# Kernel tuning notes

Measured on AMD Instinct MI355X. Metric: run time of the kernel, lower is better.

The kernel has to match this reference:

```python
import jax, jax.numpy as jnp
import numpy as np

N_HEADS = 8
D_EMBED = 512
D_HEAD = D_EMBED // N_HEADS  # used only for the scale factor, as in the source


def setup_inputs() -> dict:
    key = jax.random.key(0)
    k1, k2, k3, k4, k5 = jax.random.split(key, 5)
    B, S, D = 4, 4096, D_EMBED
    s = 1.0 / np.sqrt(D)
    return {
        "x": jax.random.normal(k1, (B, S, D), dtype=jnp.float32),
        "w_in": jax.random.normal(k2, (3 * D, D), dtype=jnp.float32) * s,
        "b_in": jax.random.normal(k3, (3 * D,), dtype=jnp.float32) * 0.01,
        "w_out": jax.random.normal(k4, (D, D), dtype=jnp.float32) * s,
        "b_out": jax.random.normal(k5, (D,), dtype=jnp.float32) * 0.01,
    }


def reference(x, w_in, b_in, w_out, b_out):
    # in_proj: torch Linear y = x @ W.T + b ; chunk into q,k,v along last dim
    qkv = jnp.einsum("bsd,ed->bse", x, w_in) + b_in  # [B,S,3D]
    q, k, v = jnp.split(qkv, 3, axis=-1)  # each [B,S,D]
    # NOTE: source never splits into heads; attention over full d_embed,
    # but scaled by sqrt(d_head) = sqrt(d_embed / n_heads).
    scores = jnp.einsum("bqd,bkd->bqk", q, k) / np.sqrt(D_HEAD)  # [B,S,S]
    weight = jax.nn.softmax(scores, axis=-1)
    out = jnp.einsum("bqk,bkd->bqd", weight, v)  # [B,S,D]
    out = jnp.einsum("bsd,ed->bse", out, w_out) + b_out
    return out
```

## Files before the change

kernel.cpp:

```cpp
#include <hip/hip_runtime.h>

typedef __bf16 bf16x8 __attribute__((ext_vector_type(8)));
typedef float f32x4 __attribute__((ext_vector_type(4)));

#define MFMA16(a, b, c) __builtin_amdgcn_mfma_f32_16x16x32_bf16(a, b, c, 0, 0, 0)
#define LOG2E 1.44269504088896340736f

__device__ __forceinline__ unsigned short f2bf(float f) {
  union { float f; unsigned u; } v; v.f = f;
  return (unsigned short)((v.u + 0x7fffu + ((v.u >> 16) & 1u)) >> 16);
}
__device__ __forceinline__ bf16x8 ld_frag(const unsigned short* p) {
  return *(const bf16x8*)p;
}
__device__ __forceinline__ void gld_lds16(const unsigned short* g, unsigned short* l) {
  __builtin_amdgcn_global_load_lds(
      (const __attribute__((address_space(1))) unsigned int*)(const void*)g,
      (__attribute__((address_space(3))) unsigned int*)(void*)l, 16, 0, 0);
}

__global__ void cvt_f2bf(const float* __restrict__ in,
                         unsigned short* __restrict__ out, int n4) {
  int i = blockIdx.x * blockDim.x + threadIdx.x;
  if (i < n4) {
    float4 v = ((const float4*)in)[i];
    ushort4 o;
    o.x = f2bf(v.x); o.y = f2bf(v.y); o.z = f2bf(v.z); o.w = f2bf(v.w);
    ((ushort4*)out)[i] = o;
  }
}

__global__ void gemm_bt(const unsigned short* __restrict__ A,
                        const unsigned short* __restrict__ B,
                        const float* __restrict__ bias,
                        float* __restrict__ outf,
                        unsigned short* __restrict__ qbuf,
                        unsigned short* __restrict__ kbuf,
                        unsigned short* __restrict__ vtbuf,
                        int M, int N, int K, int mode) {
  __shared__ alignas(16) unsigned short As[128 * 32];
  __shared__ alignas(16) unsigned short Bs[128 * 32];
  const int n0 = blockIdx.x * 128, m0 = blockIdx.y * 128;
  const int tid = threadIdx.x;
  const int l = tid & 63, w = tid >> 6;
  const int quad = l >> 4, c = l & 15;
  const int wm = (w >> 1) * 64, wn = (w & 1) * 64;

  f32x4 acc[4][4] = {};
  const int kiters = K >> 5;
  for (int kt = 0; kt < kiters; ++kt) {
    __syncthreads();
    const int kk = kt * 32 + (l & 3) * 8;
    const int row = l >> 2;
#pragma unroll
    for (int i = 0; i < 2; ++i) {
      const int rbase = i * 64 + w * 16;
      gld_lds16(&A[(size_t)(m0 + rbase + row) * K + kk], &As[rbase * 32]);
      gld_lds16(&B[(size_t)(n0 + rbase + row) * K + kk], &Bs[rbase * 32]);
    }
    __syncthreads();
    bf16x8 af[4], bfr[4];
#pragma unroll
    for (int t = 0; t < 4; ++t) {
      af[t] = ld_frag(&As[(wm + t * 16 + c) * 32 + quad * 8]);
      bfr[t] = ld_frag(&Bs[(wn + t * 16 + c) * 32 + quad * 8]);
    }
#pragma unroll
    for (int mt = 0; mt < 4; ++mt)
#pragma unroll
      for (int nt = 0; nt < 4; ++nt)
        acc[mt][nt] = MFMA16(af[mt], bfr[nt], acc[mt][nt]);
  }

#pragma unroll
  for (int nt = 0; nt < 4; ++nt) {
    const int n = n0 + wn + nt * 16 + c;
    const float bsum = bias[n];
#pragma unroll
    for (int mt = 0; mt < 4; ++mt) {
      const int mbase = m0 + wm + mt * 16 + quad * 4;
      if (mode == 0) {
#pragma unroll
        for (int r = 0; r < 4; ++r)
          outf[(size_t)(mbase + r) * N + n] = acc[mt][nt][r] + bsum;
      } else if (n < 1024) {
        unsigned short* dst = (n < 512) ? qbuf : kbuf;
        const int nn = n & 511;
#pragma unroll
        for (int r = 0; r < 4; ++r)
          dst[(size_t)(mbase + r) * 512 + nn] = f2bf(acc[mt][nt][r] + bsum);
      } else {
        const int d = n - 1024;
        const int bb = mbase >> 12, s = mbase & 4095;
        ushort4 pk;
        pk.x = f2bf(acc[mt][nt][0] + bsum);
        pk.y = f2bf(acc[mt][nt][1] + bsum);
        pk.z = f2bf(acc[mt][nt][2] + bsum);
        pk.w = f2bf(acc[mt][nt][3] + bsum);
        *(ushort4*)&vtbuf[((size_t)bb * 512 + d) * 4096 + s] = pk;
      }
    }
  }
}

#define KROW 520
#define PROW 40

__global__ __launch_bounds__(256, 2) void attn_kernel(
    const unsigned short* __restrict__ Q, const unsigned short* __restrict__ Kb,
    const unsigned short* __restrict__ Vt, unsigned short* __restrict__ part0,
    unsigned short* __restrict__ part1, float2* __restrict__ mlbuf) {
  __shared__ alignas(16) unsigned short k_lds[32 * KROW];
  __shared__ alignas(16) unsigned short v_lds[512 * 32];
  __shared__ alignas(16) unsigned short p_lds[4 * 16 * PROW];

  const int bid = blockIdx.x;
  const int xcd = bid & 7;
  const int b = xcd >> 1;
  const int half = (bid >> 3) & 1;
  const int qt = (bid >> 4) | ((xcd & 1) << 5);
  const int s0 = qt * 64;
  const int kvbase = half * 2048;
  const int tid = threadIdx.x;
  const int l = tid & 63, w = tid >> 6;
  const int quad = l >> 4, c = l & 15;
  const size_t boff = (size_t)b * 4096 * 512;

  bf16x8 qf[16];
  {
    const unsigned short* qrow = Q + boff + (size_t)(s0 + w * 16 + c) * 512;
#pragma unroll
    for (int ks = 0; ks < 16; ++ks) qf[ks] = ld_frag(&qrow[ks * 32 + quad * 8]);
  }

  f32x4 o[32] = {};
  float m_run = -1e30f, l_run = 0.f;

  const unsigned short* Kbase = Kb + boff;
  const unsigned short* Vbase = Vt + (size_t)b * 512 * 4096;

  auto stage = [&](int kv0) {
#pragma unroll
    for (int i = 0; i < 8; ++i) {
      const int row = i * 4 + w;
      gld_lds16(&Kbase[(size_t)(kv0 + row) * 512 + l * 8], &k_lds[row * KROW]);
    }
#pragma unroll
    for (int i = 0; i < 8; ++i) {
      const int dbase = (i * 4 + w) * 16;
      const int d = dbase + (l >> 2);
      const int jl = (l & 3) ^ ((d >> 1) & 3);
      gld_lds16(&Vbase[(size_t)d * 4096 + kv0 + jl * 8], &v_lds[dbase * 32]);
    }
  };

  for (int it = 0; it < 64; ++it) {
    __syncthreads();
    stage(kvbase + it * 32);
    __syncthreads();

    f32x4 sa[2][2] = {};
#pragma unroll
    for (int ks = 0; ks < 16; ++ks) {
      const unsigned short* kr = &k_lds[c * KROW + ks * 32 + quad * 8];
      bf16x8 kf0 = ld_frag(kr);
      bf16x8 kf1 = ld_frag(kr + 16 * KROW);
      sa[0][ks & 1] = MFMA16(kf0, qf[ks], sa[0][ks & 1]);
      sa[1][ks & 1] = MFMA16(kf1, qf[ks], sa[1][ks & 1]);
    }
    const f32x4 s0v = sa[0][0] + sa[0][1];
    const f32x4 s1v = sa[1][0] + sa[1][1];

    const float C1 = 0.125f * LOG2E;
    float m8 = fmaxf(fmaxf(fmaxf(s0v[0], s0v[1]), fmaxf(s0v[2], s0v[3])),
                     fmaxf(fmaxf(s1v[0], s1v[1]), fmaxf(s1v[2], s1v[3])));
    m8 = fmaxf(m8, __shfl_xor(m8, 16));
    m8 = fmaxf(m8, __shfl_xor(m8, 32));
    const float mn = fmaxf(m_run, m8);

    float p0[4], p1[4], s8 = 0.f;
#pragma unroll
    for (int r = 0; r < 4; ++r) {
      p0[r] = exp2f((s0v[r] - mn) * C1);
      p1[r] = exp2f((s1v[r] - mn) * C1);
      s8 += p0[r] + p1[r];
    }
    unsigned short* prow = &p_lds[(w * 16 + c) * PROW];
    ushort4 pk0, pk1;
    pk0.x = f2bf(p0[0]); pk0.y = f2bf(p0[1]); pk0.z = f2bf(p0[2]); pk0.w = f2bf(p0[3]);
    pk1.x = f2bf(p1[0]); pk1.y = f2bf(p1[1]); pk1.z = f2bf(p1[2]); pk1.w = f2bf(p1[3]);
    *(ushort4*)&prow[quad * 4] = pk0;
    *(ushort4*)&prow[16 + quad * 4] = pk1;

    s8 += __shfl_xor(s8, 16);
    s8 += __shfl_xor(s8, 32);

    if (__any(mn > m_run)) {
      const float alpha = exp2f((m_run - mn) * C1);
      l_run = l_run * alpha + s8;
      m_run = mn;
#pragma unroll
      for (int t = 0; t < 32; ++t) o[t] *= alpha;
    } else {
      l_run += s8;
    }

    asm volatile("s_waitcnt lgkmcnt(0)" ::: "memory");

    const bf16x8 pf = ld_frag(&p_lds[(w * 16 + c) * PROW + quad * 8]);
#pragma unroll
    for (int t = 0; t < 32; ++t) {
      const int d = t * 16 + c;
      const int jp = quad ^ ((d >> 1) & 3);
      bf16x8 vf = ld_frag(&v_lds[d * 32 + jp * 8]);
      o[t] = MFMA16(vf, pf, o[t]);
    }
  }

  unsigned short* part = half ? part1 : part0;
  const float inv = 1.0f / l_run;
  unsigned short* orow = part + boff + (size_t)(s0 + w * 16 + c) * 512;
#pragma unroll
  for (int t = 0; t < 32; ++t) {
    ushort4 pk;
    pk.x = f2bf(o[t][0] * inv);
    pk.y = f2bf(o[t][1] * inv);
    pk.z = f2bf(o[t][2] * inv);
    pk.w = f2bf(o[t][3] * inv);
    *(ushort4*)&orow[t * 16 + quad * 4] = pk;
  }
  if (quad == 0) {
    float2 ml; ml.x = m_run; ml.y = l_run;
    mlbuf[(size_t)half * 16384 + b * 4096 + s0 + w * 16 + c] = ml;
  }
}

__global__ void merge_halves(const unsigned short* __restrict__ p1,
                             const float2* __restrict__ mlbuf,
                             unsigned short* __restrict__ p0out) {
  const int i = blockIdx.x * blockDim.x + threadIdx.x;
  const int row = i >> 6;
  const float2 a = mlbuf[row];
  const float2 bb = mlbuf[16384 + row];
  const float C1 = 0.125f * LOG2E;
  const float M = fmaxf(a.x, bb.x);
  float w0 = a.y * exp2f((a.x - M) * C1);
  float w1 = bb.y * exp2f((bb.x - M) * C1);
  const float inv = 1.0f / (w0 + w1);
  w0 *= inv; w1 *= inv;
  bf16x8 v0 = *(const bf16x8*)(p0out + (size_t)i * 8);
  bf16x8 v1 = *(const bf16x8*)(p1 + (size_t)i * 8);
  ushort4 o0, o1;
  o0.x = f2bf(w0 * (float)v0[0] + w1 * (float)v1[0]);
  o0.y = f2bf(w0 * (float)v0[1] + w1 * (float)v1[1]);
  o0.z = f2bf(w0 * (float)v0[2] + w1 * (float)v1[2]);
  o0.w = f2bf(w0 * (float)v0[3] + w1 * (float)v1[3]);
  o1.x = f2bf(w0 * (float)v0[4] + w1 * (float)v1[4]);
  o1.y = f2bf(w0 * (float)v0[5] + w1 * (float)v1[5]);
  o1.z = f2bf(w0 * (float)v0[6] + w1 * (float)v1[6]);
  o1.w = f2bf(w0 * (float)v0[7] + w1 * (float)v1[7]);
  *(ushort4*)(p0out + (size_t)i * 8) = o0;
  *(ushort4*)(p0out + (size_t)i * 8 + 4) = o1;
}

extern "C" void kernel_launch(void* const* d_in, const int* in_sizes, int n_in,
                              void* d_out, int out_size, void* d_ws, size_t ws_size,
                              hipStream_t stream) {
  const float* x = (const float*)d_in[0];
  const float* w_in = (const float*)d_in[1];
  const float* b_in = (const float*)d_in[2];
  const float* w_out = (const float*)d_in[3];
  const float* b_out = (const float*)d_in[4];
  float* out = (float*)d_out;

  const size_t MTOT = (size_t)4 * 4096 * 512;
  unsigned short* q = (unsigned short*)d_ws;
  unsigned short* k = q + MTOT;
  unsigned short* vt = k + MTOT;
  unsigned short* xbf = vt + MTOT;
  unsigned short* part1 = xbf + MTOT;
  unsigned short* w_in_bf = part1 + MTOT;
  unsigned short* w_out_bf = w_in_bf + 1536 * 512;
  float2* mlbuf = (float2*)(w_out_bf + 512 * 512);

  cvt_f2bf<<<dim3((int)(MTOT / 4 / 256)), 256, 0, stream>>>(x, xbf,
                                                            (int)(MTOT / 4));
  cvt_f2bf<<<dim3(768), 256, 0, stream>>>(w_in, w_in_bf, 1536 * 512 / 4);
  cvt_f2bf<<<dim3(256), 256, 0, stream>>>(w_out, w_out_bf, 512 * 512 / 4);

  gemm_bt<<<dim3(12, 128), 256, 0, stream>>>(xbf, w_in_bf, b_in, nullptr, q, k,
                                             vt, 16384, 1536, 512, 1);
  attn_kernel<<<dim3(512), 256, 0, stream>>>(q, k, vt, xbf, part1, mlbuf);
  merge_halves<<<dim3(4096), 256, 0, stream>>>(part1, mlbuf, xbf);
  gemm_bt<<<dim3(4, 128), 256, 0, stream>>>(xbf, w_out_bf, b_out, out, nullptr,
                                            nullptr, nullptr, 16384, 512, 512,
                                            0);
}
```

Measured before the change: 444.4 us.

## Split PV work across waves by head-dim slice and prefetch K/V during compute

The P·V product is repartitioned so that each wave owns a 128-wide slice of the head dimension for all 64 query rows, instead of all 512 columns for its own 16 rows. Each V fragment is therefore loaded from LDS once and reused across four MFMAs, with P and rescale factors shared through LDS. The global-to-LDS staging of the next K tile is issued before the PV phase and the next V tile after it, overlapping loads with compute. The softmax max is also rescaled lazily, only when it grows by more than a threshold, which skips most accumulator rescales. The cost is extra block-wide barriers per iteration and extra shared-memory traffic.

After: 413.8 us. -6.9%, faster.

```diff
diff --git a/kernel.cpp b/kernel.cpp
--- a/kernel.cpp
+++ b/kernel.cpp
@@ -112,7 +112,9 @@
     unsigned short* __restrict__ part1, float2* __restrict__ mlbuf) {
   __shared__ alignas(16) unsigned short k_lds[32 * KROW];
   __shared__ alignas(16) unsigned short v_lds[512 * 32];
-  __shared__ alignas(16) unsigned short p_lds[4 * 16 * PROW];
+  __shared__ alignas(16) unsigned short p_lds[64 * PROW];
+  __shared__ float alpha_s[64];
+  __shared__ int flag_s[4];
 
   const int bid = blockIdx.x;
   const int xcd = bid & 7;
@@ -133,18 +135,20 @@
     for (int ks = 0; ks < 16; ++ks) qf[ks] = ld_frag(&qrow[ks * 32 + quad * 8]);
   }
 
-  f32x4 o[32] = {};
+  f32x4 o[8][4] = {};
   float m_run = -1e30f, l_run = 0.f;
 
   const unsigned short* Kbase = Kb + boff;
   const unsigned short* Vbase = Vt + (size_t)b * 512 * 4096;
 
-  auto stage = [&](int kv0) {
+  auto stage_k = [&](int kv0) {
 #pragma unroll
     for (int i = 0; i < 8; ++i) {
       const int row = i * 4 + w;
       gld_lds16(&Kbase[(size_t)(kv0 + row) * 512 + l * 8], &k_lds[row * KROW]);
     }
+  };
+  auto stage_v = [&](int kv0) {
 #pragma unroll
     for (int i = 0; i < 8; ++i) {
       const int dbase = (i * 4 + w) * 16;
@@ -154,9 +158,12 @@
     }
   };
 
+  stage_k(kvbase);
+  stage_v(kvbase);
+
+  const int jp8 = (quad ^ ((c >> 1) & 3)) * 8;
+
   for (int it = 0; it < 64; ++it) {
-    __syncthreads();
-    stage(kvbase + it * 32);
     __syncthreads();
 
     f32x4 sa[2][2] = {};
@@ -176,13 +183,21 @@
                      fmaxf(fmaxf(s1v[0], s1v[1]), fmaxf(s1v[2], s1v[3])));
     m8 = fmaxf(m8, __shfl_xor(m8, 16));
     m8 = fmaxf(m8, __shfl_xor(m8, 32));
-    const float mn = fmaxf(m_run, m8);
+
+    const bool need = __any(m8 - m_run > 8.0f);
+    float alpha = 1.0f;
+    if (need) {
+      const float mn = fmaxf(m_run, m8);
+      alpha = exp2f((m_run - mn) * C1);
+      m_run = mn;
+      l_run *= alpha;
+    }
 
     float p0[4], p1[4], s8 = 0.f;
 #pragma unroll
     for (int r = 0; r < 4; ++r) {
-      p0[r] = exp2f((s0v[r] - mn) * C1);
-      p1[r] = exp2f((s1v[r] - mn) * C1);
+      p0[r] = exp2f((s0v[r] - m_run) * C1);
+      p1[r] = exp2f((s1v[r] - m_run) * C1);
       s8 += p0[r] + p1[r];
     }
     unsigned short* prow = &p_lds[(w * 16 + c) * PROW];
@@ -194,44 +209,79 @@
 
     s8 += __shfl_xor(s8, 16);
     s8 += __shfl_xor(s8, 32);
-
-    if (__any(mn > m_run)) {
-      const float alpha = exp2f((m_run - mn) * C1);
-      l_run = l_run * alpha + s8;
-      m_run = mn;
-#pragma unroll
-      for (int t = 0; t < 32; ++t) o[t] *= alpha;
-    } else {
-      l_run += s8;
-    }
-
-    asm volatile("s_waitcnt lgkmcnt(0)" ::: "memory");
-
-    const bf16x8 pf = ld_frag(&p_lds[(w * 16 + c) * PROW + quad * 8]);
-#pragma unroll
-    for (int t = 0; t < 32; ++t) {
-      const int d = t * 16 + c;
-      const int jp = quad ^ ((d >> 1) & 3);
-      bf16x8 vf = ld_frag(&v_lds[d * 32 + jp * 8]);
-      o[t] = MFMA16(vf, pf, o[t]);
-    }
-  }
-
-  unsigned short* part = half ? part1 : part0;
-  const float inv = 1.0f / l_run;
-  unsigned short* orow = part + boff + (size_t)(s0 + w * 16 + c) * 512;
-#pragma unroll
-  for (int t = 0; t < 32; ++t) {
-    ushort4 pk;
-    pk.x = f2bf(o[t][0] * inv);
-    pk.y = f2bf(o[t][1] * inv);
-    pk.z = f2bf(o[t][2] * inv);
-    pk.w = f2bf(o[t][3] * inv);
-    *(ushort4*)&orow[t * 16 + quad * 4] = pk;
-  }
+    l_run += s8;
+
+    if (quad == 0) alpha_s[w * 16 + c] = alpha;
+    if (l == 0) flag_s[w] = need ? 1 : 0;
+
+    __syncthreads();
+
+    if (it + 1 < 64) stage_k(kvbase + (it + 1) * 32);
+
+    const int f0 = flag_s[0], f1 = flag_s[1], f2 = flag_s[2], f3 = flag_s[3];
+    if (f0) {
+      const float a = alpha_s[c];
+#pragma unroll
+      for (int t = 0; t < 8; ++t) o[t][0] *= a;
+    }
+    if (f1) {
+      const float a = alpha_s[16 + c];
+#pragma unroll
+      for (int t = 0; t < 8; ++t) o[t][1] *= a;
+    }
+    if (f2) {
+      const float a = alpha_s[32 + c];
+#pragma unroll
+      for (int t = 0; t < 8; ++t) o[t][2] *= a;
+    }
+    if (f3) {
+      const float a = alpha_s[48 + c];
+#pragma unroll
+      for (int t = 0; t < 8; ++t) o[t][3] *= a;
+    }
+
+    const bf16x8 pf0 = ld_frag(&p_lds[(size_t)c * PROW + quad * 8]);
+    const bf16x8 pf1 = ld_frag(&p_lds[(size_t)(16 + c) * PROW + quad * 8]);
+    const bf16x8 pf2 = ld_frag(&p_lds[(size_t)(32 + c) * PROW + quad * 8]);
+    const bf16x8 pf3 = ld_frag(&p_lds[(size_t)(48 + c) * PROW + quad * 8]);
+#pragma unroll
+    for (int t = 0; t < 8; ++t) {
+      const bf16x8 vf = ld_frag(&v_lds[(w * 128 + t * 16 + c) * 32 + jp8]);
+      o[t][0] = MFMA16(vf, pf0, o[t][0]);
+      o[t][1] = MFMA16(vf, pf1, o[t][1]);
+      o[t][2] = MFMA16(vf, pf2, o[t][2]);
+      o[t][3] = MFMA16(vf, pf3, o[t][3]);
+    }
+
+    __syncthreads();
+    if (it + 1 < 64) stage_v(kvbase + (it + 1) * 32);
+  }
+
   if (quad == 0) {
+    alpha_s[w * 16 + c] = l_run;
     float2 ml; ml.x = m_run; ml.y = l_run;
     mlbuf[(size_t)half * 16384 + b * 4096 + s0 + w * 16 + c] = ml;
+  }
+  __syncthreads();
+  const float linv0 = 1.0f / alpha_s[c];
+  const float linv1 = 1.0f / alpha_s[16 + c];
+  const float linv2 = 1.0f / alpha_s[32 + c];
+  const float linv3 = 1.0f / alpha_s[48 + c];
+
+  unsigned short* part = half ? part1 : part0;
+  unsigned short* obase = part + boff + (size_t)s0 * 512 + w * 128 + quad * 4;
+#pragma unroll
+  for (int t = 0; t < 8; ++t) {
+    const float li[4] = {linv0, linv1, linv2, linv3};
+#pragma unroll
+    for (int j = 0; j < 4; ++j) {
+      ushort4 pk;
+      pk.x = f2bf(o[t][j][0] * li[j]);
+      pk.y = f2bf(o[t][j][1] * li[j]);
+      pk.z = f2bf(o[t][j][2] * li[j]);
+      pk.w = f2bf(o[t][j][3] * li[j]);
+      *(ushort4*)&obase[(size_t)(j * 16 + c) * 512 + t * 16] = pk;
+    }
   }
 }
 
```

## Prefetch next K/V tiles during compute, keep P in registers, lazy rescale

Applied to the files above, without the earlier changes.

Splits K and V staging so the next K tile loads during the softmax/PV phase and the next V tile loads after PV, replacing the stage-then-sync loop with waitcnt-gated barriers. The probability tile is packed into the MFMA B-operand directly in registers via a permuted V^T column layout written by the projection kernel, removing the P round-trip through LDS. The running max is only updated when it grows by more than a threshold, skipping most output rescales, and s_setprio is raised around MFMA loops. This risks numeric overflow headroom assumptions and relies on the matching permutation in the V write.

After: 428.7 us. 1.04x faster.

```diff
diff --git a/kernel.cpp b/kernel.cpp
--- a/kernel.cpp
+++ b/kernel.cpp
@@ -92,19 +92,20 @@
       } else {
         const int d = n - 1024;
         const int bb = mbase >> 12, s = mbase & 4095;
+        const int cidx = (s >> 2) & 7;
+        const int sp = (s & ~31) | (((((cidx & 3) << 1) | (cidx >> 2))) << 2);
         ushort4 pk;
         pk.x = f2bf(acc[mt][nt][0] + bsum);
         pk.y = f2bf(acc[mt][nt][1] + bsum);
         pk.z = f2bf(acc[mt][nt][2] + bsum);
         pk.w = f2bf(acc[mt][nt][3] + bsum);
-        *(ushort4*)&vtbuf[((size_t)bb * 512 + d) * 4096 + s] = pk;
+        *(ushort4*)&vtbuf[((size_t)bb * 512 + d) * 4096 + sp] = pk;
       }
     }
   }
 }
 
 #define KROW 520
-#define PROW 40
 
 __global__ __launch_bounds__(256, 2) void attn_kernel(
     const unsigned short* __restrict__ Q, const unsigned short* __restrict__ Kb,
@@ -112,7 +113,6 @@
     unsigned short* __restrict__ part1, float2* __restrict__ mlbuf) {
   __shared__ alignas(16) unsigned short k_lds[32 * KROW];
   __shared__ alignas(16) unsigned short v_lds[512 * 32];
-  __shared__ alignas(16) unsigned short p_lds[4 * 16 * PROW];
 
   const int bid = blockIdx.x;
   const int xcd = bid & 7;
@@ -126,25 +126,17 @@
   const int quad = l >> 4, c = l & 15;
   const size_t boff = (size_t)b * 4096 * 512;
 
-  bf16x8 qf[16];
-  {
-    const unsigned short* qrow = Q + boff + (size_t)(s0 + w * 16 + c) * 512;
-#pragma unroll
-    for (int ks = 0; ks < 16; ++ks) qf[ks] = ld_frag(&qrow[ks * 32 + quad * 8]);
-  }
-
-  f32x4 o[32] = {};
-  float m_run = -1e30f, l_run = 0.f;
-
   const unsigned short* Kbase = Kb + boff;
   const unsigned short* Vbase = Vt + (size_t)b * 512 * 4096;
 
-  auto stage = [&](int kv0) {
+  auto stage_k = [&](int kv0) {
 #pragma unroll
     for (int i = 0; i < 8; ++i) {
       const int row = i * 4 + w;
       gld_lds16(&Kbase[(size_t)(kv0 + row) * 512 + l * 8], &k_lds[row * KROW]);
     }
+  };
+  auto stage_v = [&](int kv0) {
 #pragma unroll
     for (int i = 0; i < 8; ++i) {
       const int dbase = (i * 4 + w) * 16;
@@ -154,12 +146,30 @@
     }
   };
 
+  stage_k(kvbase);
+  stage_v(kvbase);
+
+  bf16x8 qf[16];
+  {
+    const unsigned short* qrow = Q + boff + (size_t)(s0 + w * 16 + c) * 512;
+#pragma unroll
+    for (int ks = 0; ks < 16; ++ks) qf[ks] = ld_frag(&qrow[ks * 32 + quad * 8]);
+  }
+
+  f32x4 o[32] = {};
+  float m_run = -1e30f, l_run = 0.f;
+
+  const float C1 = 0.125f * LOG2E;
+  const int jp8 = (quad ^ ((c >> 1) & 3)) * 8;
+
   for (int it = 0; it < 64; ++it) {
-    __syncthreads();
-    stage(kvbase + it * 32);
-    __syncthreads();
+    asm volatile("s_waitcnt vmcnt(8)" ::: "memory");
+    __builtin_amdgcn_sched_barrier(0);
+    __builtin_amdgcn_s_barrier();
+    __builtin_amdgcn_sched_barrier(0);
 
     f32x4 sa[2][2] = {};
+    __builtin_amdgcn_s_setprio(1);
 #pragma unroll
     for (int ks = 0; ks < 16; ++ks) {
       const unsigned short* kr = &k_lds[c * KROW + ks * 32 + quad * 8];
@@ -168,57 +178,68 @@
       sa[0][ks & 1] = MFMA16(kf0, qf[ks], sa[0][ks & 1]);
       sa[1][ks & 1] = MFMA16(kf1, qf[ks], sa[1][ks & 1]);
     }
+    __builtin_amdgcn_s_setprio(0);
     const f32x4 s0v = sa[0][0] + sa[0][1];
     const f32x4 s1v = sa[1][0] + sa[1][1];
 
-    const float C1 = 0.125f * LOG2E;
+    asm volatile("s_waitcnt vmcnt(0) lgkmcnt(0)" ::: "memory");
+    __builtin_amdgcn_sched_barrier(0);
+    __builtin_amdgcn_s_barrier();
+    __builtin_amdgcn_sched_barrier(0);
+
+    if (it + 1 < 64) stage_k(kvbase + (it + 1) * 32);
+
     float m8 = fmaxf(fmaxf(fmaxf(s0v[0], s0v[1]), fmaxf(s0v[2], s0v[3])),
                      fmaxf(fmaxf(s1v[0], s1v[1]), fmaxf(s1v[2], s1v[3])));
     m8 = fmaxf(m8, __shfl_xor(m8, 16));
     m8 = fmaxf(m8, __shfl_xor(m8, 32));
-    const float mn = fmaxf(m_run, m8);
+
+    const bool need = __any(m8 - m_run > 8.0f);
+    if (need) {
+      const float mn = fmaxf(m_run, m8);
+      const float alpha = exp2f((m_run - mn) * C1);
+      m_run = mn;
+      l_run *= alpha;
+#pragma unroll
+      for (int t = 0; t < 32; ++t) o[t] *= alpha;
+    }
 
     float p0[4], p1[4], s8 = 0.f;
 #pragma unroll
     for (int r = 0; r < 4; ++r) {
-      p0[r] = exp2f((s0v[r] - mn) * C1);
-      p1[r] = exp2f((s1v[r] - mn) * C1);
+      p0[r] = exp2f((s0v[r] - m_run) * C1);
+      p1[r] = exp2f((s1v[r] - m_run) * C1);
       s8 += p0[r] + p1[r];
     }
-    unsigned short* prow = &p_lds[(w * 16 + c) * PROW];
-    ushort4 pk0, pk1;
-    pk0.x = f2bf(p0[0]); pk0.y = f2bf(p0[1]); pk0.z = f2bf(p0[2]); pk0.w = f2bf(p0[3]);
-    pk1.x = f2bf(p1[0]); pk1.y = f2bf(p1[1]); pk1.z = f2bf(p1[2]); pk1.w = f2bf(p1[3]);
-    *(ushort4*)&prow[quad * 4] = pk0;
-    *(ushort4*)&prow[16 + quad * 4] = pk1;
-
     s8 += __shfl_xor(s8, 16);
     s8 += __shfl_xor(s8, 32);
-
-    if (__any(mn > m_run)) {
-      const float alpha = exp2f((m_run - mn) * C1);
-      l_run = l_run * alpha + s8;
-      m_run = mn;
-#pragma unroll
-      for (int t = 0; t < 32; ++t) o[t] *= alpha;
-    } else {
-      l_run += s8;
-    }
+    l_run += s8;
+
+    union { bf16x8 v; unsigned u[4]; } pfu;
+    pfu.u[0] = (unsigned)f2bf(p0[0]) | ((unsigned)f2bf(p0[1]) << 16);
+    pfu.u[1] = (unsigned)f2bf(p0[2]) | ((unsigned)f2bf(p0[3]) << 16);
+    pfu.u[2] = (unsigned)f2bf(p1[0]) | ((unsigned)f2bf(p1[1]) << 16);
+    pfu.u[3] = (unsigned)f2bf(p1[2]) | ((unsigned)f2bf(p1[3]) << 16);
+    const bf16x8 pf = pfu.v;
+
+    __builtin_amdgcn_s_setprio(1);
+#pragma unroll
+    for (int t = 0; t < 32; ++t) {
+      const bf16x8 vf = ld_frag(&v_lds[(t * 16 + c) * 32 + jp8]);
+      o[t] = MFMA16(vf, pf, o[t]);
+    }
+    __builtin_amdgcn_s_setprio(0);
 
     asm volatile("s_waitcnt lgkmcnt(0)" ::: "memory");
-
-    const bf16x8 pf = ld_frag(&p_lds[(w * 16 + c) * PROW + quad * 8]);
-#pragma unroll
-    for (int t = 0; t < 32; ++t) {
-      const int d = t * 16 + c;
-      const int jp = quad ^ ((d >> 1) & 3);
-      bf16x8 vf = ld_frag(&v_lds[d * 32 + jp * 8]);
-      o[t] = MFMA16(vf, pf, o[t]);
-    }
-  }
-
+    __builtin_amdgcn_sched_barrier(0);
+    __builtin_amdgcn_s_barrier();
+    __builtin_amdgcn_sched_barrier(0);
+
+    if (it + 1 < 64) stage_v(kvbase + (it + 1) * 32);
+  }
+
+  const float inv = 1.0f / l_run;
   unsigned short* part = half ? part1 : part0;
-  const float inv = 1.0f / l_run;
   unsigned short* orow = part + boff + (size_t)(s0 + w * 16 + c) * 512;
 #pragma unroll
   for (int t = 0; t < 32; ++t) {
```
